# Kernel tuning notes

Measured on AMD Instinct MI355X. Metric: run time of the kernel, lower is better.

Reference implementation:

```python
import jax, jax.numpy as jnp
import numpy as np

OUT_SIZE = 7          # pooled output resolution
SR = 2                # sampling_ratio (samples per bin side)
SCALES = (0.25, 0.125, 0.0625, 0.03125)   # FPN P2..P5 -> min_level=2, max_level=5
MIN_LEVEL, MAX_LEVEL = 2, 5
CANON_SIZE, CANON_LEVEL = 224.0, 4.0


def _roi_align(feat, boxes, bidx, scale):
    """ROIAlignV2 (aligned=True), fixed sampling_ratio.
    feat: [N,C,H,W]; boxes: [M,4] (x1,y1,x2,y2 in image coords); bidx: [M] int.
    Returns [M,C,OUT_SIZE,OUT_SIZE]."""
    N, C, H, W = feat.shape
    featT = jnp.transpose(feat, (0, 2, 3, 1))  # [N,H,W,C] for channel-last gathers
    # aligned=True: half-pixel offset
    x1 = boxes[:, 0] * scale - 0.5
    y1 = boxes[:, 1] * scale - 0.5
    x2 = boxes[:, 2] * scale - 0.5
    y2 = boxes[:, 3] * scale - 0.5
    bw = (x2 - x1) / OUT_SIZE
    bh = (y2 - y1) / OUT_SIZE
    # flattened per-bin sample offsets: for bin i, sample j -> i + (j+0.5)/SR
    k = jnp.arange(OUT_SIZE * SR)
    off = (k // SR).astype(feat.dtype) + ((k % SR).astype(feat.dtype) + 0.5) / SR  # [P]
    ys = y1[:, None] + off[None, :] * bh[:, None]  # [M,P]
    xs = x1[:, None] + off[None, :] * bw[:, None]  # [M,P]
    # validity (torchvision semantics: zero outside [-1, size])
    vy = (ys >= -1.0) & (ys <= H)
    vx = (xs >= -1.0) & (xs <= W)
    valid = vy[:, :, None] & vx[:, None, :]        # [M,P,P]
    y = jnp.clip(ys, 0.0, H - 1.0)
    x = jnp.clip(xs, 0.0, W - 1.0)
    y0 = jnp.floor(y).astype(jnp.int32)
    x0 = jnp.floor(x).astype(jnp.int32)
    y1i = jnp.minimum(y0 + 1, H - 1)
    x1i = jnp.minimum(x0 + 1, W - 1)
    ly = y - y0.astype(y.dtype)
    lx = x - x0.astype(x.dtype)
    hy, hx = 1.0 - ly, 1.0 - lx

    def gather(yi, xi):  # -> [M,P,P,C]
        return featT[bidx[:, None, None], yi[:, :, None], xi[:, None, :]]

    val = (hy[:, :, None] * hx[:, None, :])[..., None] * gather(y0, x0)
    val = val + (hy[:, :, None] * lx[:, None, :])[..., None] * gather(y0, x1i)
    val = val + (ly[:, :, None] * hx[:, None, :])[..., None] * gather(y1i, x0)
    val = val + (ly[:, :, None] * lx[:, None, :])[..., None] * gather(y1i, x1i)
    val = jnp.where(valid[..., None], val, 0.0)
    M = boxes.shape[0]
    # average SRxSR samples per bin
    val = val.reshape(M, OUT_SIZE, SR, OUT_SIZE, SR, C).mean(axis=(2, 4))
    return jnp.transpose(val, (0, 3, 1, 2))  # [M,C,7,7]


def _pool(feats, boxes):
    N, R, _ = boxes.shape
    b = boxes.reshape(-1, 4)                        # [M,4], M = N*R (pooler-format concat)
    bidx = jnp.repeat(jnp.arange(N), R)             # batch index column
    # assign_boxes_to_levels: log2 area bucketing
    sizes = jnp.sqrt(jnp.maximum((b[:, 2] - b[:, 0]) * (b[:, 3] - b[:, 1]), 0.0))
    lvl = jnp.floor(CANON_LEVEL + jnp.log2(sizes / CANON_SIZE + 1e-8))
    lvl = jnp.clip(lvl, MIN_LEVEL, MAX_LEVEL).astype(jnp.int32) - MIN_LEVEL  # [M] in [0,3]
    out = jnp.zeros((b.shape[0], feats[0].shape[1], OUT_SIZE, OUT_SIZE), feats[0].dtype)
    for l, (f, s) in enumerate(zip(feats, SCALES)):
        pooled = _roi_align(f, b, bidx, s)
        out = out + jnp.where((lvl == l)[:, None, None, None], pooled, 0.0)
    return out


def setup_inputs() -> dict:
    key = jax.random.key(0)
    ks = jax.random.split(key, 6)
    N, R, IMG = 2, 512, 1024.0
    shapes = [(2, 256, 256, 256), (2, 256, 128, 128), (2, 256, 64, 64), (2, 256, 32, 32)]
    feats = [jax.random.normal(ks[i], s, dtype=jnp.float32) for i, s in enumerate(shapes)]
    # box sizes log-uniform in [32, 800] px so all 4 levels get boxes
    wh = jnp.exp(jax.random.uniform(ks[4], (N, R, 2), minval=jnp.log(32.0), maxval=jnp.log(800.0)))
    cxy = jax.random.uniform(ks[5], (N, R, 2), minval=0.0, maxval=IMG)
    x1y1 = jnp.clip(cxy - wh / 2, 0.0, IMG)
    x2y2 = jnp.clip(cxy + wh / 2, 0.0, IMG)
    boxes = jnp.concatenate([x1y1, x2y2], axis=-1)  # [N,R,4]
    return {"feat0": feats[0], "feat1": feats[1], "feat2": feats[2], "feat3": feats[3], "boxes": boxes}


def reference(feat0, feat1, feat2, feat3, boxes):
    return _pool((feat0, feat1, feat2, feat3), boxes)
```

## Files before the change

kernel.cpp:

```cpp
#include <hip/hip_runtime.h>

#define OUT 7
#define CCH 256

__device__ __forceinline__ unsigned short f2bf(float f) {
    union { float f; unsigned int u; } v; v.f = f;
    unsigned int r = (v.u + 0x7FFFu + ((v.u >> 16) & 1u)) >> 16;
    return (unsigned short)r;
}
__device__ __forceinline__ float bf2f_lo(unsigned int u) {
    union { unsigned int u; float f; } v; v.u = u << 16;
    return v.f;
}
__device__ __forceinline__ float bf2f_hi(unsigned int u) {
    union { unsigned int u; float f; } v; v.u = u & 0xFFFF0000u;
    return v.f;
}

__global__ __launch_bounds__(256) void roi_pool_naive(
    const float* __restrict__ f0, const float* __restrict__ f1,
    const float* __restrict__ f2, const float* __restrict__ f3,
    const float* __restrict__ boxes, float* __restrict__ out,
    int M, int R)
{
    int idx = blockIdx.x * blockDim.x + threadIdx.x;
    int total = M * CCH * OUT * OUT;
    if (idx >= total) return;
    int pw = idx % OUT;
    int ph = (idx / OUT) % OUT;
    int c  = (idx / (OUT * OUT)) % CCH;
    int m  = idx / (OUT * OUT * CCH);
    int n  = m / R;
    const float bx1 = boxes[m * 4 + 0], by1 = boxes[m * 4 + 1];
    const float bx2 = boxes[m * 4 + 2], by2 = boxes[m * 4 + 3];
    float sz  = sqrtf(fmaxf((bx2 - bx1) * (by2 - by1), 0.0f));
    int lvl = (int)floorf(4.0f + log2f(sz / 224.0f + 1e-8f));
    lvl = min(max(lvl, 2), 5) - 2;
    const float* feat; int H, W; float scale;
    switch (lvl) {
        case 0:  feat = f0; H = 256; W = 256; scale = 0.25f;    break;
        case 1:  feat = f1; H = 128; W = 128; scale = 0.125f;   break;
        case 2:  feat = f2; H = 64;  W = 64;  scale = 0.0625f;  break;
        default: feat = f3; H = 32;  W = 32;  scale = 0.03125f; break;
    }
    const float* fp = feat + (size_t)(n * CCH + c) * (size_t)(H * W);
    float x1 = bx1 * scale - 0.5f, y1 = by1 * scale - 0.5f;
    float x2 = bx2 * scale - 0.5f, y2 = by2 * scale - 0.5f;
    float bw = (x2 - x1) * (1.0f / OUT), bh = (y2 - y1) * (1.0f / OUT);
    float acc = 0.0f;
    #pragma unroll
    for (int iy = 0; iy < 2; iy++) {
        float ys = y1 + ((float)ph + ((float)iy + 0.5f) * 0.5f) * bh;
        bool vy = (ys >= -1.0f) && (ys <= (float)H);
        float y = fminf(fmaxf(ys, 0.0f), (float)(H - 1));
        int y0 = (int)y;
        int y1i = min(y0 + 1, H - 1);
        float ly = y - (float)y0, hy = 1.0f - ly;
        #pragma unroll
        for (int ix = 0; ix < 2; ix++) {
            float xs = x1 + ((float)pw + ((float)ix + 0.5f) * 0.5f) * bw;
            bool vx = (xs >= -1.0f) && (xs <= (float)W);
            float x = fminf(fmaxf(xs, 0.0f), (float)(W - 1));
            int x0 = (int)x;
            int x1ii = min(x0 + 1, W - 1);
            float lx = x - (float)x0, hx = 1.0f - lx;
            if (vy && vx) {
                acc += hy * hx * fp[y0 * W + x0]  + hy * lx * fp[y0 * W + x1ii]
                     + ly * hx * fp[y1i * W + x0] + ly * lx * fp[y1i * W + x1ii];
            }
        }
    }
    out[idx] = acc * 0.25f;
}

__global__ __launch_bounds__(256) void transpose_all(
    const float* __restrict__ f0, const float* __restrict__ f1,
    const float* __restrict__ f2, const float* __restrict__ f3,
    unsigned short* __restrict__ o0, unsigned short* __restrict__ o1,
    unsigned short* __restrict__ o2, unsigned short* __restrict__ o3,
    int N)
{
    __shared__ unsigned int lds[CCH][32];

    int rem = blockIdx.x;
    const int nb0 = 1024 * N;
    const int nb1 = 256 * N;
    const int nb2 = 64 * N;
    const float* in; unsigned short* op; int HW, lshift;
    if (rem < nb0)        { in = f0; op = o0; HW = 65536; lshift = 10; }
    else { rem -= nb0;
      if (rem < nb1)      { in = f1; op = o1; HW = 16384; lshift = 8;  }
      else { rem -= nb1;
        if (rem < nb2)    { in = f2; op = o2; HW = 4096;  lshift = 6;  }
        else { rem -= nb2;  in = f3; op = o3; HW = 1024;  lshift = 4;  }
      }
    }
    int hw0 = (rem & ((1 << lshift) - 1)) << 6;
    int n   = rem >> lshift;

    int t  = threadIdx.x;
    int tx = t & 15;
    int ty = t >> 4;

    const float4* in4 = (const float4*)(in + (size_t)n * CCH * HW);
    #pragma unroll
    for (int j = 0; j < 16; j++) {
        int c = ty + 16 * j;
        float4 v = in4[((size_t)c * HW + (size_t)hw0) / 4 + tx];
        unsigned int u0 = (unsigned int)f2bf(v.x) | ((unsigned int)f2bf(v.y) << 16);
        unsigned int u1 = (unsigned int)f2bf(v.z) | ((unsigned int)f2bf(v.w) << 16);
        int e   = 2 * (c >> 3) + 8 * (c & 3);
        int col = (2 * tx + e) & 31;
        *(uint2*)(&lds[c][col]) = make_uint2(u0, u1);
    }
    __syncthreads();

    int txc  = t & 31;
    int row8 = t >> 5;
    unsigned short* ob = op + (size_t)n * HW * CCH;
    #pragma unroll
    for (int p = 0; p < 8; p++) {
        int hwl = 8 * p + row8;
        int hwp = hwl >> 1;
        int sel = hwl & 1;
        unsigned int w[4];
        #pragma unroll
        for (int kk = 0; kk < 4; kk++) {
            int ca = 8 * txc + 2 * kk;
            int cb = ca + 1;
            unsigned int ua = lds[ca][(hwp + 2 * txc + 8 * ((2 * kk) & 3)) & 31];
            unsigned int ub = lds[cb][(hwp + 2 * txc + 8 * ((2 * kk + 1) & 3)) & 31];
            unsigned int ha = sel ? (ua >> 16)          : (ua & 0xFFFFu);
            unsigned int hb = sel ? (ub & 0xFFFF0000u)  : (ub << 16);
            w[kk] = ha | hb;
        }
        uint4 vv; vv.x = w[0]; vv.y = w[1]; vv.z = w[2]; vv.w = w[3];
        ((uint4*)(ob + (size_t)(hw0 + hwl) * CCH))[txc] = vv;
    }
}

__global__ __launch_bounds__(128) void roi_pool_cl2(
    const unsigned short* __restrict__ t0, const unsigned short* __restrict__ t1,
    const unsigned short* __restrict__ t2, const unsigned short* __restrict__ t3,
    const float* __restrict__ boxes, float* __restrict__ out, int M, int R)
{
    int bx = blockIdx.x;
    int m, ph;
    if ((M & 7) == 0) {
        int q = bx / 56, rem = bx - q * 56;
        ph = rem >> 3;
        m  = q * 8 + (rem & 7);
    } else {
        m = bx / OUT; ph = bx % OUT;
    }
    int t = threadIdx.x;
    int n = m / R;

    const float bx1 = boxes[m * 4 + 0], by1 = boxes[m * 4 + 1];
    const float bx2 = boxes[m * 4 + 2], by2 = boxes[m * 4 + 3];
    float sz  = sqrtf(fmaxf((bx2 - bx1) * (by2 - by1), 0.0f));
    int lvl = (int)floorf(4.0f + log2f(sz / 224.0f + 1e-8f));
    lvl = min(max(lvl, 2), 5) - 2;

    const unsigned short* feat; int H, W; float scale;
    switch (lvl) {
        case 0:  feat = t0; H = 256; W = 256; scale = 0.25f;    break;
        case 1:  feat = t1; H = 128; W = 128; scale = 0.125f;   break;
        case 2:  feat = t2; H = 64;  W = 64;  scale = 0.0625f;  break;
        default: feat = t3; H = 32;  W = 32;  scale = 0.03125f; break;
    }
    const unsigned short* fb = feat + (size_t)n * H * W * CCH;

    float x1 = bx1 * scale - 0.5f, y1 = by1 * scale - 0.5f;
    float x2 = bx2 * scale - 0.5f, y2 = by2 * scale - 0.5f;
    float bw = (x2 - x1) * (1.0f / OUT), bh = (y2 - y1) * (1.0f / OUT);

    int   r0[2], r1[2];
    float lyv[2], hyv[2];
    bool  vyv[2];
    #pragma unroll
    for (int iy = 0; iy < 2; iy++) {
        float ys = y1 + ((float)ph + ((float)iy + 0.5f) * 0.5f) * bh;
        vyv[iy] = (ys >= -1.0f) && (ys <= (float)H);
        float y = fminf(fmaxf(ys, 0.0f), (float)(H - 1));
        int y0 = (int)y;
        int y1i = min(y0 + 1, H - 1);
        lyv[iy] = y - (float)y0;
        hyv[iy] = 1.0f - lyv[iy];
        r0[iy] = y0 * W * CCH;
        r1[iy] = y1i * W * CCH;
    }

    float accA[OUT];
    float accB[OUT];
    #pragma unroll
    for (int pw = 0; pw < OUT; pw++) {
        float aA = 0.0f, aB = 0.0f;
        #pragma unroll
        for (int ix = 0; ix < 2; ix++) {
            float xs = x1 + ((float)pw + ((float)ix + 0.5f) * 0.5f) * bw;
            bool vx = (xs >= -1.0f) && (xs <= (float)W);
            float x = fminf(fmaxf(xs, 0.0f), (float)(W - 1));
            int x0 = (int)x;
            int x1i = min(x0 + 1, W - 1);
            float lx = x - (float)x0;
            float hx = 1.0f - lx;
            int c0o = x0 * CCH;
            int c1o = x1i * CCH;
            #pragma unroll
            for (int iy = 0; iy < 2; iy++) {
                if (vyv[iy] && vx) {
                    const unsigned int* p00 = (const unsigned int*)(fb + __builtin_amdgcn_readfirstlane(r0[iy] + c0o));
                    const unsigned int* p01 = (const unsigned int*)(fb + __builtin_amdgcn_readfirstlane(r0[iy] + c1o));
                    const unsigned int* p10 = (const unsigned int*)(fb + __builtin_amdgcn_readfirstlane(r1[iy] + c0o));
                    const unsigned int* p11 = (const unsigned int*)(fb + __builtin_amdgcn_readfirstlane(r1[iy] + c1o));
                    unsigned int u00 = p00[t], u01 = p01[t];
                    unsigned int u10 = p10[t], u11 = p11[t];
                    float w00 = hyv[iy] * hx, w01 = hyv[iy] * lx;
                    float w10 = lyv[iy] * hx, w11 = lyv[iy] * lx;
                    aA += w00 * bf2f_lo(u00) + w01 * bf2f_lo(u01)
                        + w10 * bf2f_lo(u10) + w11 * bf2f_lo(u11);
                    aB += w00 * bf2f_hi(u00) + w01 * bf2f_hi(u01)
                        + w10 * bf2f_hi(u10) + w11 * bf2f_hi(u11);
                }
            }
        }
        accA[pw] = aA * 0.25f;
        accB[pw] = aB * 0.25f;
    }

    float* obA = out + (size_t)m * (CCH * OUT * OUT) + (size_t)(2 * t) * (OUT * OUT) + ph * OUT;
    float* obB = obA + (OUT * OUT);
    #pragma unroll
    for (int k = 0; k < OUT; k++) obA[k] = accA[k];
    #pragma unroll
    for (int k = 0; k < OUT; k++) obB[k] = accB[k];
}

extern "C" void kernel_launch(void* const* d_in, const int* in_sizes, int n_in,
                              void* d_out, int out_size, void* d_ws, size_t ws_size,
                              hipStream_t stream) {
    const float* f0    = (const float*)d_in[0];
    const float* f1    = (const float*)d_in[1];
    const float* f2    = (const float*)d_in[2];
    const float* f3    = (const float*)d_in[3];
    const float* boxes = (const float*)d_in[4];
    float* out = (float*)d_out;

    int N = in_sizes[0] / (CCH * 256 * 256);
    int M = in_sizes[4] / 4;
    int R = M / N;

    size_t nshorts = (size_t)N * CCH * (65536 + 16384 + 4096 + 1024);
    if (ws_size >= nshorts * sizeof(unsigned short)) {
        unsigned short* t0 = (unsigned short*)d_ws;
        unsigned short* t1 = t0 + (size_t)N * CCH * 65536;
        unsigned short* t2 = t1 + (size_t)N * CCH * 16384;
        unsigned short* t3 = t2 + (size_t)N * CCH * 4096;
        int tblocks = (1024 + 256 + 64 + 16) * N;
        transpose_all<<<tblocks, 256, 0, stream>>>(f0, f1, f2, f3, t0, t1, t2, t3, N);
        roi_pool_cl2<<<M * OUT, 128, 0, stream>>>(t0, t1, t2, t3, boxes, out, M, R);
    } else {
        int total = M * CCH * OUT * OUT;
        roi_pool_naive<<<(total + 255) / 256, 256, 0, stream>>>(f0, f1, f2, f3, boxes, out, M, R);
    }
}
```

Baseline: 296.1 us.

## Retile NCHW-to-NHWC bf16 transpose into 64-channel by 256-pixel tiles with batched loads

The transpose kernel now handles tiles of 64 channels by 256 spatial positions instead of all 256 channels by 64 positions. Each wave reads 1 KB contiguous per channel row, and all 16 float4 loads are issued before any conversion to raise memory-level parallelism. A new LDS swizzle keeps bank conflicts low. The trade-off is that each output row write is only 128 bytes per pixel (8 threads × 16B), not a full 512-byte channel row, and the new tile indexing must be correct for all four levels.

```diff
diff --git a/kernel.cpp b/kernel.cpp
--- a/kernel.cpp
+++ b/kernel.cpp
@@ -80,62 +80,70 @@
     unsigned short* __restrict__ o2, unsigned short* __restrict__ o3,
     int N)
 {
-    __shared__ unsigned int lds[CCH][32];
+    __shared__ unsigned int lds[64][128];
 
     int rem = blockIdx.x;
     const int nb0 = 1024 * N;
     const int nb1 = 256 * N;
     const int nb2 = 64 * N;
-    const float* in; unsigned short* op; int HW, lshift;
-    if (rem < nb0)        { in = f0; op = o0; HW = 65536; lshift = 10; }
+    const float* in; unsigned short* op; int HW, shift;
+    if (rem < nb0)        { in = f0; op = o0; HW = 65536; shift = 8; }
     else { rem -= nb0;
-      if (rem < nb1)      { in = f1; op = o1; HW = 16384; lshift = 8;  }
+      if (rem < nb1)      { in = f1; op = o1; HW = 16384; shift = 6; }
       else { rem -= nb1;
-        if (rem < nb2)    { in = f2; op = o2; HW = 4096;  lshift = 6;  }
-        else { rem -= nb2;  in = f3; op = o3; HW = 1024;  lshift = 4;  }
+        if (rem < nb2)    { in = f2; op = o2; HW = 4096;  shift = 4; }
+        else { rem -= nb2;  in = f3; op = o3; HW = 1024;  shift = 2; }
       }
     }
-    int hw0 = (rem & ((1 << lshift) - 1)) << 6;
-    int n   = rem >> lshift;
-
-    int t  = threadIdx.x;
-    int tx = t & 15;
-    int ty = t >> 4;
-
-    const float4* in4 = (const float4*)(in + (size_t)n * CCH * HW);
-    #pragma unroll
-    for (int j = 0; j < 16; j++) {
-        int c = ty + 16 * j;
-        float4 v = in4[((size_t)c * HW + (size_t)hw0) / 4 + tx];
-        unsigned int u0 = (unsigned int)f2bf(v.x) | ((unsigned int)f2bf(v.y) << 16);
-        unsigned int u1 = (unsigned int)f2bf(v.z) | ((unsigned int)f2bf(v.w) << 16);
-        int e   = 2 * (c >> 3) + 8 * (c & 3);
-        int col = (2 * tx + e) & 31;
+    int hw0 = (rem & ((1 << shift) - 1)) << 8;
+    int c0  = ((rem >> shift) & 3) << 6;
+    int n   = rem >> (shift + 2);
+
+    int t = threadIdx.x;
+    int w = t >> 6;
+    int l = t & 63;
+
+    const float4* in4 = (const float4*)(in + ((size_t)n * CCH + c0) * HW);
+    float4 v[16];
+    #pragma unroll
+    for (int i = 0; i < 16; i++) {
+        int c = 16 * w + i;
+        v[i] = in4[((size_t)c * HW + hw0) / 4 + l];
+    }
+    #pragma unroll
+    for (int i = 0; i < 16; i++) {
+        int c = 16 * w + i;
+        unsigned int u0 = (unsigned int)f2bf(v[i].x) | ((unsigned int)f2bf(v[i].y) << 16);
+        unsigned int u1 = (unsigned int)f2bf(v[i].z) | ((unsigned int)f2bf(v[i].w) << 16);
+        int rot = (2 * c + 4 * (c >> 3)) & 127;
+        int col = (2 * l + rot) & 127;
         *(uint2*)(&lds[c][col]) = make_uint2(u0, u1);
     }
     __syncthreads();
 
-    int txc  = t & 31;
-    int row8 = t >> 5;
-    unsigned short* ob = op + (size_t)n * HW * CCH;
+    int tl = t & 7;
+    int tr = t >> 3;
+    unsigned short* ob = op + (size_t)n * HW * CCH + c0;
     #pragma unroll
     for (int p = 0; p < 8; p++) {
-        int hwl = 8 * p + row8;
+        int hwl = p * 32 + tr;
         int hwp = hwl >> 1;
         int sel = hwl & 1;
-        unsigned int w[4];
+        unsigned int wv[4];
         #pragma unroll
         for (int kk = 0; kk < 4; kk++) {
-            int ca = 8 * txc + 2 * kk;
+            int ca = 8 * tl + 2 * kk;
             int cb = ca + 1;
-            unsigned int ua = lds[ca][(hwp + 2 * txc + 8 * ((2 * kk) & 3)) & 31];
-            unsigned int ub = lds[cb][(hwp + 2 * txc + 8 * ((2 * kk + 1) & 3)) & 31];
-            unsigned int ha = sel ? (ua >> 16)          : (ua & 0xFFFFu);
-            unsigned int hb = sel ? (ub & 0xFFFF0000u)  : (ub << 16);
-            w[kk] = ha | hb;
+            int rota = (2 * ca + 4 * (ca >> 3)) & 127;
+            int rotb = (2 * cb + 4 * (cb >> 3)) & 127;
+            unsigned int ua = lds[ca][(hwp + rota) & 127];
+            unsigned int ub = lds[cb][(hwp + rotb) & 127];
+            unsigned int ha = sel ? (ua >> 16)         : (ua & 0xFFFFu);
+            unsigned int hb = sel ? (ub & 0xFFFF0000u) : (ub << 16);
+            wv[kk] = ha | hb;
         }
-        uint4 vv; vv.x = w[0]; vv.y = w[1]; vv.z = w[2]; vv.w = w[3];
-        ((uint4*)(ob + (size_t)(hw0 + hwl) * CCH))[txc] = vv;
+        uint4 vv; vv.x = wv[0]; vv.y = wv[1]; vv.z = wv[2]; vv.w = wv[3];
+        ((uint4*)(ob + (size_t)(hw0 + hwl) * CCH))[tl] = vv;
     }
 }
 
```

Result: no change. 294.2 us (-0.7%).
